# Optimization experiments

Hardware: AMD Instinct MI355X
Metric: run time of the kernel (lower is better)

The kernel has to match this reference:

```python
import jax, jax.numpy as jnp
import numpy as np

B, S, HID, NH = 8, 1024, 1024, 16
DH = HID // NH
ZERO = 1e-8  # undefined repo constant, assumed small epsilon


def setup_inputs() -> dict:
    key = jax.random.key(0)
    ks = jax.random.split(key, 14)
    sc = 1.0 / np.sqrt(HID)
    inp = {
        "Q": jax.random.normal(ks[0], (B, S, HID), jnp.float32),
        "K": jax.random.normal(ks[1], (B, S, HID), jnp.float32),
        "V": jax.random.normal(ks[2], (B, S, HID), jnp.float32),
        "Q_mask": jax.random.randint(ks[3], (B, S), 0, 2).astype(jnp.float32),
        "K_mask": jax.random.randint(ks[4], (B, S), 0, 2).astype(jnp.float32),
        "Wq": jax.random.normal(ks[5], (HID, HID), jnp.float32) * sc,
        "bq": jnp.zeros((HID,), jnp.float32),
        "Wk": jax.random.normal(ks[6], (HID, HID), jnp.float32) * sc,
        "bk": jnp.zeros((HID,), jnp.float32),
        "Wv": jax.random.normal(ks[7], (HID, HID), jnp.float32) * sc,
        "bv": jnp.zeros((HID,), jnp.float32),
        "Wo": jax.random.normal(ks[8], (HID, HID), jnp.float32) * sc,
        "bo": jnp.zeros((HID,), jnp.float32),
    }
    return inp


def _heads(x):  # [B,S,HID] -> [B,NH,S,DH]
    b, s, _ = x.shape
    return x.reshape(b, s, NH, DH).transpose(0, 2, 1, 3)


def reference(Q, K, V, Q_mask, K_mask, Wq, bq, Wk, bk, Wv, bv, Wo, bo):
    q = _heads(Q @ Wq.T + bq)
    k = _heads(K @ Wk.T + bk)
    v = _heads(V @ Wv.T + bv)
    # NOTE: original divides by head_size**(-0.5) == multiply by sqrt(DH)
    scores = jnp.einsum("bhqd,bhkd->bhqk", q, k) / (DH ** (-0.5))
    mask = Q_mask[:, :, None] * K_mask[:, None, :]  # [B,Sq,Sk]
    probs = jax.nn.softmax(scores, axis=-1)
    probs = jnp.where(mask[:, None, :, :] == 0, 0.0, probs)
    probs = probs / jnp.sum(probs + ZERO, axis=-1, keepdims=True)
    ctx = jnp.einsum("bhqk,bhkd->bqhd", probs, v).reshape(Q.shape[0], Q.shape[1], HID)
    return ctx @ Wo.T + bo
```

## Files before the change

kernel.cpp:

```cpp
#include <hip/hip_runtime.h>
#include <math.h>

constexpr int Bc   = 8;
constexpr int Sc   = 1024;
constexpr int HIDc = 1024;
constexpr int NHc  = 16;
constexpr int DHc  = 64;
constexpr int Mc   = Bc * Sc;
constexpr int Kc2  = 1024;
constexpr float SCALE    = 8.0f;
constexpr float EPS_TERM = 1024.0f * 1e-8f;

typedef short s16x8 __attribute__((ext_vector_type(8)));
typedef float f32x4 __attribute__((ext_vector_type(4)));

__device__ __forceinline__ ushort f2bf(float f) {
  unsigned u = __float_as_uint(f);
  u += 0x7FFFu + ((u >> 16) & 1u);
  return (ushort)(u >> 16);
}
__device__ __forceinline__ float bf2f(ushort h) {
  return __uint_as_float(((unsigned)h) << 16);
}
__device__ __forceinline__ unsigned pk2bf(float a, float b) {
  return (unsigned)f2bf(a) | ((unsigned)f2bf(b) << 16);
}

__device__ __forceinline__ void gl_lds16(const ushort* g, ushort* l) {
  __builtin_amdgcn_global_load_lds(
      (const __attribute__((address_space(1))) void*)g,
      (__attribute__((address_space(3))) void*)l, 16, 0, 0);
}

__device__ __forceinline__ void split8(const float4 v0, const float4 v1,
                                       s16x8& hi, s16x8& lo) {
  const float f[8] = {v0.x, v0.y, v0.z, v0.w, v1.x, v1.y, v1.z, v1.w};
  ushort h[8], l[8];
#pragma unroll
  for (int i = 0; i < 8; i++) {
    h[i] = f2bf(f[i]);
    l[i] = f2bf(f[i] - bf2f(h[i]));
  }
#pragma unroll
  for (int i = 0; i < 8; i++) { hi[i] = (short)h[i]; lo[i] = (short)l[i]; }
}

__global__ __launch_bounds__(256) void cvt_weights(
    const float4* __restrict__ Wq, const float4* __restrict__ Wk,
    const float4* __restrict__ Wv, const float4* __restrict__ Wo,
    ushort4* __restrict__ Wqh, ushort4* __restrict__ Wql,
    ushort4* __restrict__ Wkh, ushort4* __restrict__ Wkl,
    ushort4* __restrict__ Wvh, ushort4* __restrict__ Woh, int n4w)
{
  const int bpseg = n4w / 256;
  const int seg   = blockIdx.x / bpseg;
  const int li    = (blockIdx.x - seg * bpseg) * 256 + threadIdx.x;
  if (li >= n4w) return;
  if (seg == 0) {
    const float4 v = Wq[li];
    ushort4 h, l;
    h.x = f2bf(v.x); l.x = f2bf(v.x - bf2f(h.x));
    h.y = f2bf(v.y); l.y = f2bf(v.y - bf2f(h.y));
    h.z = f2bf(v.z); l.z = f2bf(v.z - bf2f(h.z));
    h.w = f2bf(v.w); l.w = f2bf(v.w - bf2f(h.w));
    Wqh[li] = h; Wql[li] = l;
  } else if (seg == 1) {
    const float4 v = Wk[li];
    ushort4 h, l;
    h.x = f2bf(v.x); l.x = f2bf(v.x - bf2f(h.x));
    h.y = f2bf(v.y); l.y = f2bf(v.y - bf2f(h.y));
    h.z = f2bf(v.z); l.z = f2bf(v.z - bf2f(h.z));
    h.w = f2bf(v.w); l.w = f2bf(v.w - bf2f(h.w));
    Wkh[li] = h; Wkl[li] = l;
  } else {
    const float4 v = (seg == 2) ? Wv[li] : Wo[li];
    ushort4 h;
    h.x = f2bf(v.x); h.y = f2bf(v.y); h.z = f2bf(v.z); h.w = f2bf(v.w);
    if (seg == 2) Wvh[li] = h; else Woh[li] = h;
  }
}

__global__ __launch_bounds__(256, 3) void qkv_gemm(
    const float* __restrict__ Qf, const float* __restrict__ Kf,
    const float* __restrict__ Vf,
    const ushort* __restrict__ Wqh, const ushort* __restrict__ Wql,
    const ushort* __restrict__ Wkh, const ushort* __restrict__ Wkl,
    const ushort* __restrict__ Wvh,
    const float* __restrict__ bq, const float* __restrict__ bk,
    const float* __restrict__ bv,
    ushort* __restrict__ qhi, ushort* __restrict__ qlo,
    ushort* __restrict__ khi, ushort* __restrict__ klo,
    ushort* __restrict__ vt)
{
  __shared__ ushort AhL[4096];
  __shared__ ushort BhL[4096];
  __shared__ ushort AlL[4096];
  __shared__ ushort BlL[4096];

  const int z = blockIdx.z;
  const bool split = (z < 2);
  const float*  Af = (z == 0) ? Qf : (z == 1) ? Kf : Vf;
  const ushort* Bh = (z == 0) ? Wqh : (z == 1) ? Wkh : Wvh;
  const ushort* Bl = (z == 0) ? Wql : Wkl;
  const float* bias = (z == 0) ? bq : (z == 1) ? bk : bv;

  const int t    = threadIdx.x;
  const int w    = t >> 6;
  const int ln   = t & 63;
  const int col  = ln & 15;
  const int quad = ln >> 4;
  const int wm   = w >> 1, wn = w & 1;
  const int m0   = blockIdx.y * 128;
  const int n0   = blockIdx.x * 128;

  f32x4 acc[4][4] = {};

  const int sA = w * 128;

  for (int k0 = 0; k0 < Kc2; k0 += 32) {
    float4 av[2][2];
#pragma unroll
    for (int j = 0; j < 2; j++) {
      const int s = sA + j * 64 + ln;
      const int r = s & 127, c = s >> 7;
      const float4* ga = (const float4*)(Af + (size_t)(m0 + r) * Kc2 + k0 + c * 8);
      av[j][0] = ga[0];
      av[j][1] = ga[1];
    }

    __syncthreads();

#pragma unroll
    for (int j = 0; j < 2; j++) {
      const int s = sA + j * 64 + ln;
      const int r = s & 127, c = s >> 7;
      const size_t goB = (size_t)(n0 + r) * Kc2 + k0 + c * 8;
      gl_lds16(Bh + goB, &BhL[(size_t)(sA + j * 64) * 8]);
      if (split) gl_lds16(Bl + goB, &BlL[(size_t)(sA + j * 64) * 8]);
    }
#pragma unroll
    for (int j = 0; j < 2; j++) {
      const int s = sA + j * 64 + ln;
      s16x8 hi, lo;
      split8(av[j][0], av[j][1], hi, lo);
      *(s16x8*)&AhL[(size_t)s * 8] = hi;
      if (split) *(s16x8*)&AlL[(size_t)s * 8] = lo;
    }
    __syncthreads();

    s16x8 a_h[4], b_h[4], a_l[4], b_l[4];
#pragma unroll
    for (int i = 0; i < 4; i++) {
      const int ai = (quad * 128 + wm * 64 + i * 16 + col) * 8;
      const int bi = (quad * 128 + wn * 64 + i * 16 + col) * 8;
      a_h[i] = *(const s16x8*)&AhL[ai];
      b_h[i] = *(const s16x8*)&BhL[bi];
      if (split) {
        a_l[i] = *(const s16x8*)&AlL[ai];
        b_l[i] = *(const s16x8*)&BlL[bi];
      }
    }
#pragma unroll
    for (int i = 0; i < 4; i++)
#pragma unroll
      for (int jj = 0; jj < 4; jj++) {
        acc[i][jj] = __builtin_amdgcn_mfma_f32_16x16x32_bf16(a_h[i], b_h[jj], acc[i][jj], 0, 0, 0);
        if (split) {
          acc[i][jj] = __builtin_amdgcn_mfma_f32_16x16x32_bf16(a_h[i], b_l[jj], acc[i][jj], 0, 0, 0);
          acc[i][jj] = __builtin_amdgcn_mfma_f32_16x16x32_bf16(a_l[i], b_h[jj], acc[i][jj], 0, 0, 0);
        }
      }
  }

  const int mb = m0 + wm * 64;
  const int nb = n0 + wn * 64;
  ushort* Ch = (z == 0) ? qhi : khi;
  ushort* Cl = (z == 0) ? qlo : klo;
#pragma unroll
  for (int i = 0; i < 4; i++)
#pragma unroll
    for (int jj = 0; jj < 4; jj++) {
      const int n  = nb + jj * 16 + col;
      const float bvv = bias[n];
#pragma unroll
      for (int r = 0; r < 4; r++) {
        const int m   = mb + i * 16 + quad * 4 + r;
        const float v = acc[i][jj][r] + bvv;
        const int b_ = m >> 10, s = m & (Sc - 1);
        const int h_ = n >> 6,  d = n & (DHc - 1);
        if (split) {
          const size_t off = (((size_t)b_ * NHc + h_) * Sc + s) * DHc + d;
          const ushort hb = f2bf(v);
          Ch[off] = hb;
          Cl[off] = f2bf(v - bf2f(hb));
        } else {
          const size_t off = (((size_t)b_ * NHc + h_) * DHc + d) * Sc + s;
          vt[off] = f2bf(v);
        }
      }
    }
}

__global__ __launch_bounds__(256, 3) void o_gemm(
    const ushort* __restrict__ Ag, const ushort* __restrict__ Bg,
    const float* __restrict__ bias, float* __restrict__ C)
{
  __shared__ ushort AhL[4096];
  __shared__ ushort BhL[4096];

  const int t    = threadIdx.x;
  const int w    = t >> 6;
  const int ln   = t & 63;
  const int col  = ln & 15;
  const int quad = ln >> 4;
  const int wm   = w >> 1, wn = w & 1;
  const int m0   = blockIdx.y * 128;
  const int n0   = blockIdx.x * 128;

  f32x4 acc[4][4] = {};
  const int sA = w * 128;

  for (int k0 = 0; k0 < Kc2; k0 += 32) {
    __syncthreads();
#pragma unroll
    for (int j = 0; j < 2; j++) {
      const int s = sA + j * 64 + ln;
      const int r = s & 127, c = s >> 7;
      gl_lds16(Ag + (size_t)(m0 + r) * Kc2 + k0 + c * 8, &AhL[(size_t)(sA + j * 64) * 8]);
      gl_lds16(Bg + (size_t)(n0 + r) * Kc2 + k0 + c * 8, &BhL[(size_t)(sA + j * 64) * 8]);
    }
    __syncthreads();

    s16x8 a_h[4], b_h[4];
#pragma unroll
    for (int i = 0; i < 4; i++) {
      a_h[i] = *(const s16x8*)&AhL[(quad * 128 + wm * 64 + i * 16 + col) * 8];
      b_h[i] = *(const s16x8*)&BhL[(quad * 128 + wn * 64 + i * 16 + col) * 8];
    }
#pragma unroll
    for (int i = 0; i < 4; i++)
#pragma unroll
      for (int jj = 0; jj < 4; jj++)
        acc[i][jj] = __builtin_amdgcn_mfma_f32_16x16x32_bf16(a_h[i], b_h[jj], acc[i][jj], 0, 0, 0);
  }

  const int mb = m0 + wm * 64;
  const int nb = n0 + wn * 64;
#pragma unroll
  for (int i = 0; i < 4; i++)
#pragma unroll
    for (int jj = 0; jj < 4; jj++) {
      const int n  = nb + jj * 16 + col;
      const float bvv = bias[n];
#pragma unroll
      for (int r = 0; r < 4; r++) {
        const int m = mb + i * 16 + quad * 4 + r;
        C[(size_t)m * HIDc + n] = acc[i][jj][r] + bvv;
      }
    }
}

constexpr int LDP = 72;

__global__ __launch_bounds__(256, 4) void attn_mfma(
    const ushort* __restrict__ qhi, const ushort* __restrict__ qlo,
    const ushort* __restrict__ khi, const ushort* __restrict__ klo,
    const ushort* __restrict__ vt,  const float* __restrict__ Qm,
    const float* __restrict__ Km,   ushort* __restrict__ ctx)
{
  __shared__ ushort KhiL[4096];
  __shared__ ushort KloL[4096];
  __shared__ ushort VtL [4096];
  __shared__ ushort PmL [64 * LDP];
  __shared__ float  kmL[64];

  const int t    = threadIdx.x;
  const int w    = t >> 6;
  const int ln   = t & 63;
  const int col  = ln & 15;
  const int quad = ln >> 4;

  const int id  = blockIdx.x;
  const int xcd = id & 7;
  const int j   = id >> 3;
  const int bh  = xcd * 16 + (j >> 4);
  const int qt  = j & 15;
  const int b   = bh >> 4;
  const int h   = bh & 15;

  const int qbase = qt * 64 + w * 16;
  const size_t headoff = (size_t)bh * Sc * DHc;

  s16x8 qh0, qh1, ql0, ql1;
  {
    const size_t ro = headoff + (size_t)(qbase + col) * DHc + quad * 8;
    qh0 = *(const s16x8*)(qhi + ro);
    qh1 = *(const s16x8*)(qhi + ro + 32);
    ql0 = *(const s16x8*)(qlo + ro);
    ql1 = *(const s16x8*)(qlo + ro + 32);
  }

  f32x4 OT[4] = {{0,0,0,0},{0,0,0,0},{0,0,0,0},{0,0,0,0}};
  float mrow = -INFINITY;
  float Zp = 0.0f, Zmp = 0.0f;

  for (int k0 = 0; k0 < Sc; k0 += 64) {
    __syncthreads();
#pragma unroll
    for (int jj = 0; jj < 2; jj++) {
      const int c = jj * 4 + w;
      const size_t gk = headoff + (size_t)(k0 + ln) * DHc + c * 8;
      const size_t gv = headoff + (size_t)ln * Sc + k0 + c * 8;
      gl_lds16(khi + gk, &KhiL[c * 512]);
      gl_lds16(klo + gk, &KloL[c * 512]);
      gl_lds16(vt  + gv, &VtL [c * 512]);
    }
    if (t < 64) kmL[t] = Km[b * Sc + k0 + t];
    __syncthreads();

    float s[4][4];
#pragma unroll
    for (int ks = 0; ks < 4; ks++) {
      const int base0 = (quad * 64 + ks * 16 + col) * 8;
      const int base1 = ((quad + 4) * 64 + ks * 16 + col) * 8;
      const s16x8 kh0 = *(const s16x8*)&KhiL[base0];
      const s16x8 kh1 = *(const s16x8*)&KhiL[base1];
      const s16x8 kl0 = *(const s16x8*)&KloL[base0];
      const s16x8 kl1 = *(const s16x8*)&KloL[base1];
      f32x4 a = {0,0,0,0};
      a = __builtin_amdgcn_mfma_f32_16x16x32_bf16(kh0, qh0, a, 0, 0, 0);
      a = __builtin_amdgcn_mfma_f32_16x16x32_bf16(kh1, qh1, a, 0, 0, 0);
      a = __builtin_amdgcn_mfma_f32_16x16x32_bf16(kh0, ql0, a, 0, 0, 0);
      a = __builtin_amdgcn_mfma_f32_16x16x32_bf16(kh1, ql1, a, 0, 0, 0);
      a = __builtin_amdgcn_mfma_f32_16x16x32_bf16(kl0, qh0, a, 0, 0, 0);
      a = __builtin_amdgcn_mfma_f32_16x16x32_bf16(kl1, qh1, a, 0, 0, 0);
#pragma unroll
      for (int r = 0; r < 4; r++) s[ks][r] = a[r] * SCALE;
    }

    float tmax = s[0][0];
#pragma unroll
    for (int ks = 0; ks < 4; ks++)
#pragma unroll
      for (int r = 0; r < 4; r++) tmax = fmaxf(tmax, s[ks][r]);
    tmax = fmaxf(tmax, __shfl_xor(tmax, 16, 64));
    tmax = fmaxf(tmax, __shfl_xor(tmax, 32, 64));

    const float mn    = fmaxf(mrow, tmax);
    const float alpha = __expf(mrow - mn);
    mrow = mn;

    float ps = 0.0f, pms = 0.0f;
    const int prow = (w * 16 + col) * LDP;
#pragma unroll
    for (int ks = 0; ks < 4; ks++) {
      const float4 km4 = *(const float4*)&kmL[ks * 16 + quad * 4];
      const float p0 = __expf(s[ks][0] - mn), p1 = __expf(s[ks][1] - mn);
      const float p2 = __expf(s[ks][2] - mn), p3 = __expf(s[ks][3] - mn);
      const float q0 = p0 * km4.x, q1 = p1 * km4.y, q2 = p2 * km4.z, q3 = p3 * km4.w;
      ps  += (p0 + p1) + (p2 + p3);
      pms += (q0 + q1) + (q2 + q3);
      uint2 pv;
      pv.x = pk2bf(q0, q1);
      pv.y = pk2bf(q2, q3);
      *(uint2*)&PmL[prow + ks * 16 + quad * 4] = pv;
    }
    Zp  = Zp  * alpha + ps;
    Zmp = Zmp * alpha + pms;
#pragma unroll
    for (int dt = 0; dt < 4; dt++) OT[dt] *= alpha;

    const s16x8 p0 = *(const s16x8*)&PmL[prow + quad * 8];
    const s16x8 p1 = *(const s16x8*)&PmL[prow + 32 + quad * 8];
#pragma unroll
    for (int dt = 0; dt < 4; dt++) {
      const s16x8 a0 = *(const s16x8*)&VtL[(quad * 64 + dt * 16 + col) * 8];
      const s16x8 a1 = *(const s16x8*)&VtL[((quad + 4) * 64 + dt * 16 + col) * 8];
      OT[dt] = __builtin_amdgcn_mfma_f32_16x16x32_bf16(a0, p0, OT[dt], 0, 0, 0);
      OT[dt] = __builtin_amdgcn_mfma_f32_16x16x32_bf16(a1, p1, OT[dt], 0, 0, 0);
    }
  }

  Zp  += __shfl_xor(Zp,  16, 64);  Zp  += __shfl_xor(Zp,  32, 64);
  Zmp += __shfl_xor(Zmp, 16, 64);  Zmp += __shfl_xor(Zmp, 32, 64);

  const int q     = qbase + col;
  const float qmv = Qm[b * Sc + q];
  const float rden = (qmv != 0.0f) ? 1.0f / (Zmp + EPS_TERM * Zp) : 0.0f;

  ushort* crow = ctx + (size_t)(b * Sc + q) * HIDc + h * DHc + quad * 4;
#pragma unroll
  for (int dt = 0; dt < 4; dt++) {
    uint2 ov;
    ov.x = pk2bf(OT[dt][0] * rden, OT[dt][1] * rden);
    ov.y = pk2bf(OT[dt][2] * rden, OT[dt][3] * rden);
    *(uint2*)(crow + dt * 16) = ov;
  }
}

extern "C" void kernel_launch(void* const* d_in, const int* in_sizes, int n_in,
                              void* d_out, int out_size, void* d_ws, size_t ws_size,
                              hipStream_t stream)
{
  const float* Q  = (const float*)d_in[0];
  const float* K  = (const float*)d_in[1];
  const float* V  = (const float*)d_in[2];
  const float* Qm = (const float*)d_in[3];
  const float* Km = (const float*)d_in[4];
  const float* Wq = (const float*)d_in[5];
  const float* bq = (const float*)d_in[6];
  const float* Wk = (const float*)d_in[7];
  const float* bk = (const float*)d_in[8];
  const float* Wv = (const float*)d_in[9];
  const float* bv = (const float*)d_in[10];
  const float* Wo = (const float*)d_in[11];
  const float* bo = (const float*)d_in[12];
  float* out = (float*)d_out;

  const size_t NEL = (size_t)Mc * HIDc;
  const size_t WEL = (size_t)HIDc * HIDc;

  ushort* Wqh = (ushort*)d_ws;
  ushort* Wql = Wqh + WEL;
  ushort* Wkh = Wql + WEL;
  ushort* Wkl = Wkh + WEL;
  ushort* Wvh = Wkl + WEL;
  ushort* Woh = Wvh + WEL;
  ushort* qhi = Woh + WEL;
  ushort* qlo = qhi + NEL;
  ushort* khi = qlo + NEL;
  ushort* klo = khi + NEL;
  ushort* vt  = klo + NEL;
  ushort* ctx = vt  + NEL;

  const int n4w = (int)(WEL / 4);

  cvt_weights<<<4 * (n4w / 256), 256, 0, stream>>>(
      (const float4*)Wq, (const float4*)Wk, (const float4*)Wv, (const float4*)Wo,
      (ushort4*)Wqh, (ushort4*)Wql, (ushort4*)Wkh, (ushort4*)Wkl,
      (ushort4*)Wvh, (ushort4*)Woh, n4w);

  dim3 gqkv(HIDc / 128, Mc / 128, 3);
  qkv_gemm<<<gqkv, 256, 0, stream>>>(Q, K, V,
      Wqh, Wql, Wkh, Wkl, Wvh, bq, bk, bv, qhi, qlo, khi, klo, vt);

  attn_mfma<<<Bc * NHc * (Sc / 64), 256, 0, stream>>>(qhi, qlo, khi, klo, vt, Qm, Km, ctx);

  dim3 gg(HIDc / 128, Mc / 128);
  o_gemm<<<gg, 256, 0, stream>>>(ctx, Woh, bo, out);
}
```

Measured before the change: 531.3 us.

## Pre-split fp32 inputs to bf16 hi/lo in separate pass; async LDS loads in QKV GEMM

Adds a cvt_inputs kernel that converts Q/K/V from fp32 into bf16 hi/lo (hi only for V) buffers once, so the QKV GEMM loads A tiles straight into LDS through the same global-to-LDS path already used for the weights. Before, each tile was converted in registers, and because every row tile reloads and re-splits the same A data across the N-dimension blocks, that conversion was repeated. It also raises the launch-bounds occupancy hint from 3 to 4 and reuses the split-input buffer for ctx. The cost is an extra kernel launch and extra global traffic to write and read the split buffers.

```diff
diff --git a/kernel.cpp b/kernel.cpp
--- a/kernel.cpp
+++ b/kernel.cpp
@@ -80,9 +80,38 @@
   }
 }
 
-__global__ __launch_bounds__(256, 3) void qkv_gemm(
-    const float* __restrict__ Qf, const float* __restrict__ Kf,
-    const float* __restrict__ Vf,
+__global__ __launch_bounds__(256) void cvt_inputs(
+    const float4* __restrict__ Qf, const float4* __restrict__ Kf,
+    const float4* __restrict__ Vf,
+    s16x8* __restrict__ Qsh, s16x8* __restrict__ Qsl,
+    s16x8* __restrict__ Ksh, s16x8* __restrict__ Ksl,
+    s16x8* __restrict__ Vsh, int n8)
+{
+  const int bpseg = n8 / 256;
+  const int seg   = blockIdx.x / bpseg;
+  const int li    = (blockIdx.x - seg * bpseg) * 256 + threadIdx.x;
+  if (li >= n8) return;
+  const float4* src = (seg == 0) ? Qf : (seg == 1) ? Kf : Vf;
+  const float4 v0 = src[2 * li];
+  const float4 v1 = src[2 * li + 1];
+  if (seg < 2) {
+    s16x8 hi, lo;
+    split8(v0, v1, hi, lo);
+    if (seg == 0) { Qsh[li] = hi; Qsl[li] = lo; }
+    else          { Ksh[li] = hi; Ksl[li] = lo; }
+  } else {
+    const float f[8] = {v0.x, v0.y, v0.z, v0.w, v1.x, v1.y, v1.z, v1.w};
+    s16x8 hi;
+#pragma unroll
+    for (int i = 0; i < 8; i++) hi[i] = (short)f2bf(f[i]);
+    Vsh[li] = hi;
+  }
+}
+
+__global__ __launch_bounds__(256, 4) void qkv_gemm(
+    const ushort* __restrict__ Qsh, const ushort* __restrict__ Qsl,
+    const ushort* __restrict__ Ksh, const ushort* __restrict__ Ksl,
+    const ushort* __restrict__ Vsh,
     const ushort* __restrict__ Wqh, const ushort* __restrict__ Wql,
     const ushort* __restrict__ Wkh, const ushort* __restrict__ Wkl,
     const ushort* __restrict__ Wvh,
@@ -99,7 +128,8 @@
 
   const int z = blockIdx.z;
   const bool split = (z < 2);
-  const float*  Af = (z == 0) ? Qf : (z == 1) ? Kf : Vf;
+  const ushort* Ah = (z == 0) ? Qsh : (z == 1) ? Ksh : Vsh;
+  const ushort* Al = (z == 0) ? Qsl : Ksl;
   const ushort* Bh = (z == 0) ? Wqh : (z == 1) ? Wkh : Wvh;
   const ushort* Bl = (z == 0) ? Wql : Wkl;
   const float* bias = (z == 0) ? bq : (z == 1) ? bk : bv;
@@ -118,33 +148,20 @@
   const int sA = w * 128;
 
   for (int k0 = 0; k0 < Kc2; k0 += 32) {
-    float4 av[2][2];
+    __syncthreads();
 #pragma unroll
     for (int j = 0; j < 2; j++) {
       const int s = sA + j * 64 + ln;
       const int r = s & 127, c = s >> 7;
-      const float4* ga = (const float4*)(Af + (size_t)(m0 + r) * Kc2 + k0 + c * 8);
-      av[j][0] = ga[0];
-      av[j][1] = ga[1];
-    }
-
-    __syncthreads();
-
-#pragma unroll
-    for (int j = 0; j < 2; j++) {
-      const int s = sA + j * 64 + ln;
-      const int r = s & 127, c = s >> 7;
+      const int ldst = (sA + j * 64) * 8;
+      const size_t goA = (size_t)(m0 + r) * Kc2 + k0 + c * 8;
       const size_t goB = (size_t)(n0 + r) * Kc2 + k0 + c * 8;
-      gl_lds16(Bh + goB, &BhL[(size_t)(sA + j * 64) * 8]);
-      if (split) gl_lds16(Bl + goB, &BlL[(size_t)(sA + j * 64) * 8]);
-    }
-#pragma unroll
-    for (int j = 0; j < 2; j++) {
-      const int s = sA + j * 64 + ln;
-      s16x8 hi, lo;
-      split8(av[j][0], av[j][1], hi, lo);
-      *(s16x8*)&AhL[(size_t)s * 8] = hi;
-      if (split) *(s16x8*)&AlL[(size_t)s * 8] = lo;
+      gl_lds16(Ah + goA, &AhL[ldst]);
+      gl_lds16(Bh + goB, &BhL[ldst]);
+      if (split) {
+        gl_lds16(Al + goA, &AlL[ldst]);
+        gl_lds16(Bl + goB, &BlL[ldst]);
+      }
     }
     __syncthreads();
 
@@ -426,12 +443,17 @@
   ushort* Wkl = Wkh + WEL;
   ushort* Wvh = Wkl + WEL;
   ushort* Woh = Wvh + WEL;
-  ushort* qhi = Woh + WEL;
+  ushort* Qsh = Woh + WEL;
+  ushort* Qsl = Qsh + NEL;
+  ushort* Ksh = Qsl + NEL;
+  ushort* Ksl = Ksh + NEL;
+  ushort* Vsh = Ksl + NEL;
+  ushort* qhi = Vsh + NEL;
   ushort* qlo = qhi + NEL;
   ushort* khi = qlo + NEL;
   ushort* klo = khi + NEL;
   ushort* vt  = klo + NEL;
-  ushort* ctx = vt  + NEL;
+  ushort* ctx = Qsh;
 
   const int n4w = (int)(WEL / 4);
 
@@ -440,8 +462,14 @@
       (ushort4*)Wqh, (ushort4*)Wql, (ushort4*)Wkh, (ushort4*)Wkl,
       (ushort4*)Wvh, (ushort4*)Woh, n4w);
 
+  const int n8 = (int)(NEL / 8);
+  cvt_inputs<<<3 * (n8 / 256), 256, 0, stream>>>(
+      (const float4*)Q, (const float4*)K, (const float4*)V,
+      (s16x8*)Qsh, (s16x8*)Qsl, (s16x8*)Ksh, (s16x8*)Ksl, (s16x8*)Vsh, n8);
+
   dim3 gqkv(HIDc / 128, Mc / 128, 3);
-  qkv_gemm<<<gqkv, 256, 0, stream>>>(Q, K, V,
+  qkv_gemm<<<gqkv, 256, 0, stream>>>(
+      Qsh, Qsl, Ksh, Ksl, Vsh,
       Wqh, Wql, Wkh, Wkl, Wvh, bq, bk, bv, qhi, qlo, khi, klo, vt);
 
   attn_mfma<<<Bc * NHc * (Sc / 64), 256, 0, stream>>>(qhi, qlo, khi, klo, vt, Qm, Km, ctx);
```

Result: slower. 1.070 ms (+101.4%).
